# Kernel optimization log

Hardware: AMD Instinct MI355X
Metric: run time of the kernel (lower is better)

## Reference

```python
import jax, jax.numpy as jnp
import numpy as np

B, C, CI, H, W = 8, 256, 64, 64, 64  # batch, in_channels, inter_channels, spatial


def conv1x1(x, w, b):
    # x: [B,C,H,W], w: [O,C] (1x1 kernel), b: [O]
    return jnp.einsum('bchw,oc->bohw', x, w) + b[None, :, None, None]


def setup_inputs() -> dict:
    key = jax.random.key(0)
    ks = jax.random.split(key, 9)
    s_in = 1.0 / np.sqrt(C)
    s_ci = 1.0 / np.sqrt(CI)
    return {
        'x': jax.random.normal(ks[0], (B, C, H, W), dtype=jnp.float32),
        'g_w': jax.random.uniform(ks[1], (CI, C), jnp.float32, -s_in, s_in),
        'g_b': jax.random.uniform(ks[2], (CI,), jnp.float32, -s_in, s_in),
        'theta_w': jax.random.uniform(ks[3], (CI, C), jnp.float32, -s_in, s_in),
        'theta_b': jax.random.uniform(ks[4], (CI,), jnp.float32, -s_in, s_in),
        'phi_w': jax.random.uniform(ks[5], (CI, C), jnp.float32, -s_in, s_in),
        'phi_b': jax.random.uniform(ks[6], (CI,), jnp.float32, -s_in, s_in),
        'w_w': jax.random.uniform(ks[7], (C, CI), jnp.float32, -s_ci, s_ci),
        'w_b': jax.random.uniform(ks[8], (C,), jnp.float32, -s_ci, s_ci),
    }


def reference(x, g_w, g_b, theta_w, theta_b, phi_w, phi_b, w_w, w_b):
    b, c, h, w = x.shape
    n = h * w
    # 1x1 conv projections, flattened over spatial positions -> [B, N, CI]
    g_x = conv1x1(x, g_w, g_b).reshape(b, CI, n).transpose(0, 2, 1)
    theta_x = conv1x1(x, theta_w, theta_b).reshape(b, CI, n).transpose(0, 2, 1)
    phi_x = conv1x1(x, phi_w, phi_b).reshape(b, CI, n)  # [B, CI, N]
    # Full non-scaled attention over spatial positions
    f = jnp.einsum('bnc,bcm->bnm', theta_x, phi_x)       # [B, N, N]
    f_div_c = jax.nn.softmax(f, axis=-1)
    y = jnp.einsum('bnm,bmc->bnc', f_div_c, g_x)         # [B, N, CI]
    y = y.transpose(0, 2, 1).reshape(b, CI, h, w)
    w_y = conv1x1(y, w_w, w_b)                            # [B, C, H, W]
    return w_y + x
```

## Files before the change

### kernel.cpp

```cpp
#include <hip/hip_runtime.h>
#include <hip/hip_bf16.h>

#define B_  8
#define C_  256
#define CI_ 64
#define N_  4096
#define KSPLIT 2
#define KTILES (N_ / 64 / KSPLIT)

typedef short short8  __attribute__((ext_vector_type(8)));
typedef short sh4     __attribute__((ext_vector_type(4)));
typedef float floatx4 __attribute__((ext_vector_type(4)));

__device__ __forceinline__ unsigned short f2bf(float f) {
    unsigned u = __builtin_bit_cast(unsigned, f);
    u += 0x7FFFu + ((u >> 16) & 1u);
    return (unsigned short)(u >> 16);
}

__device__ __forceinline__ unsigned pk2(float a, float b) {
#if __has_builtin(__builtin_amdgcn_cvt_pk_bf16_f32)
    auto r = __builtin_amdgcn_cvt_pk_bf16_f32(a, b);
    return __builtin_bit_cast(unsigned, r);
#else
    return (unsigned)f2bf(a) | ((unsigned)f2bf(b) << 16);
#endif
}

__device__ __forceinline__ floatx4 mfma32(short8 a, short8 b, floatx4 c) {
    return __builtin_amdgcn_mfma_f32_16x16x32_bf16(a, b, c, 0, 0, 0);
}
__device__ __forceinline__ floatx4 mfma16(sh4 a, sh4 b, floatx4 c) {
#if __has_builtin(__builtin_amdgcn_mfma_f32_16x16x16bf16_1k)
    return __builtin_amdgcn_mfma_f32_16x16x16bf16_1k(a, b, c, 0, 0, 0);
#else
    floatx4 d;
    asm("v_mfma_f32_16x16x16_bf16 %0, %1, %2, %3" : "=v"(d) : "v"(a), "v"(b), "v"(c));
    return d;
#endif
}

__global__ __launch_bounds__(256) void proj_kernel(
    const float* __restrict__ x,
    const float* __restrict__ wg, const float* __restrict__ bg,
    const float* __restrict__ wt, const float* __restrict__ bt,
    const float* __restrict__ wp, const float* __restrict__ bp,
    unsigned short* __restrict__ gws,
    unsigned short* __restrict__ tws,
    unsigned short* __restrict__ pws)
{
    constexpr int WS = 40;
    constexpr int GS = 72;
    __shared__ __align__(16) unsigned short wsl[2][192 * WS];
    __shared__ __align__(16) unsigned short gt[64 * GS];

    const int t    = threadIdx.x;
    const int lane = t & 63;
    const int w    = t >> 6;
    const int l15  = lane & 15;
    const int quad = lane >> 4;
    const int n0   = blockIdx.x * 64;
    const int b    = blockIdx.y;

    floatx4 acc[12];
#pragma unroll
    for (int ot = 0; ot < 12; ++ot) { floatx4 z = {0.f, 0.f, 0.f, 0.f}; acc[ot] = z; }

    const int nA = n0 + w * 16 + l15;
    const float* xbase = x + (size_t)b * C_ * N_ + nA;

#pragma unroll
    for (int it = 0; it < 6; ++it) {
        int u = t + it * 256;
        int row = u >> 3, c4 = u & 7;
        const float* src = (row < 64)  ? (wg + row * C_)
                         : (row < 128) ? (wt + (row - 64) * C_)
                                       : (wp + (row - 128) * C_);
        float4 v = *(const float4*)(src + c4 * 4);
        uint2 uu = { pk2(v.x, v.y), pk2(v.z, v.w) };
        *(uint2*)&wsl[0][row * WS + c4 * 4] = uu;
    }
    float xv[8];
#pragma unroll
    for (int j = 0; j < 8; ++j) xv[j] = xbase[(size_t)(quad * 8 + j) * N_];
    __syncthreads();

    for (int kk = 0; kk < 8; ++kk) {
        uint4 au = { pk2(xv[0], xv[1]), pk2(xv[2], xv[3]),
                     pk2(xv[4], xv[5]), pk2(xv[6], xv[7]) };
        short8 af = __builtin_bit_cast(short8, au);

        float nx[8];
        if (kk < 7) {
#pragma unroll
            for (int j = 0; j < 8; ++j)
                nx[j] = xbase[(size_t)((kk + 1) * 32 + quad * 8 + j) * N_];
#pragma unroll
            for (int it = 0; it < 6; ++it) {
                int u = t + it * 256;
                int row = u >> 3, c4 = u & 7;
                const float* src = (row < 64)  ? (wg + row * C_)
                                 : (row < 128) ? (wt + (row - 64) * C_)
                                               : (wp + (row - 128) * C_);
                float4 v = *(const float4*)(src + (kk + 1) * 32 + c4 * 4);
                uint2 uu = { pk2(v.x, v.y), pk2(v.z, v.w) };
                *(uint2*)&wsl[(kk + 1) & 1][row * WS + c4 * 4] = uu;
            }
        }

#pragma unroll
        for (int ot = 0; ot < 12; ++ot) {
            short8 bf = *(const short8*)&wsl[kk & 1][(ot * 16 + l15) * WS + quad * 8];
            acc[ot] = mfma32(af, bf, acc[ot]);
        }
        __syncthreads();
#pragma unroll
        for (int j = 0; j < 8; ++j) xv[j] = nx[j];
    }

#pragma unroll
    for (int ot = 0; ot < 12; ++ot) {
        const int oc = ot * 16 + l15;
        const float bias = (ot < 4) ? bg[oc] : (ot < 8) ? bt[oc - 64] : bp[oc - 128];
        if (ot < 4) {
#pragma unroll
            for (int r = 0; r < 4; ++r)
                gt[oc * GS + w * 16 + quad * 4 + r] = f2bf(acc[ot][r] + bias);
        } else {
            unsigned short* dst = (ot < 8) ? tws : pws;
            const int ci = (ot < 8) ? (oc - 64) : (oc - 128);
#pragma unroll
            for (int r = 0; r < 4; ++r) {
                int n = n0 + w * 16 + quad * 4 + r;
                dst[((size_t)b * N_ + n) * CI_ + ci] = f2bf(acc[ot][r] + bias);
            }
        }
    }
    __syncthreads();
#pragma unroll
    for (int it = 0; it < 2; ++it) {
        int u = t + it * 256;
        int ci = u >> 3, n8 = u & 7;
        uint4 v = *(const uint4*)&gt[ci * GS + n8 * 8];
        *(uint4*)(gws + ((size_t)b * CI_ + ci) * N_ + n0 + n8 * 8) = v;
    }
}

__global__ __launch_bounds__(256, 4) void attn_kernel(
    const unsigned short* __restrict__ gws,
    const unsigned short* __restrict__ tws,
    const unsigned short* __restrict__ pws,
    float* __restrict__ Opart,
    float* __restrict__ lpart)
{
    constexpr int LDW = 72;
    __shared__ __align__(16) unsigned short Ks[2][64 * LDW];
    __shared__ __align__(16) unsigned short Vs[2][64 * LDW];

    const int t    = threadIdx.x;
    const int lane = t & 63;
    const int w    = t >> 6;
    const int l15  = lane & 15;
    const int quad = lane >> 4;
    const int b    = blockIdx.x;
    const int q0   = blockIdx.y * 64;
    const int sp   = blockIdx.z;

    const int srow = t >> 3;
    const int sc8  = t & 7;

    const uint4* kbase = (const uint4*)(pws + ((size_t)b * N_ + sp * (N_ / KSPLIT)) * CI_);
    const unsigned short* vbase =
        gws + ((size_t)b * CI_ + srow) * N_ + sp * (N_ / KSPLIT) + sc8 * 8;

    short8 qf[2];
    {
        const unsigned short* qrow = tws + ((size_t)b * N_ + q0 + w * 16 + l15) * CI_;
        qf[0] = *(const short8*)(qrow + quad * 8);
        qf[1] = *(const short8*)(qrow + 32 + quad * 8);
    }

    {
        uint4 k0 = kbase[t];
        uint4 k1 = kbase[t + 256];
        uint4 v0 = *(const uint4*)(vbase);
        uint4 v1 = *(const uint4*)(vbase + 32 * N_);
        *(uint4*)&Ks[0][srow * LDW + sc8 * 8]        = k0;
        *(uint4*)&Ks[0][(srow + 32) * LDW + sc8 * 8] = k1;
        *(uint4*)&Vs[0][srow * LDW + sc8 * 8]        = v0;
        *(uint4*)&Vs[0][(srow + 32) * LDW + sc8 * 8] = v1;
    }
    __syncthreads();

    sh4 ones4;
#pragma unroll
    for (int j = 0; j < 4; ++j) ones4[j] = (short)0x3F80;

    floatx4 Oacc[4], lacc;
    { floatx4 z = {0.f, 0.f, 0.f, 0.f}; lacc = z;
#pragma unroll
      for (int f = 0; f < 4; ++f) Oacc[f] = z; }

    const float LOG2E = 1.4426950408889634f;

    for (int j = 0; j < KTILES; ++j) {
        const int p  = j & 1;
        const int jn = (j + 1) & (KTILES - 1);

        uint4 pk0 = kbase[jn * 512 + t];
        uint4 pk1 = kbase[jn * 512 + t + 256];
        uint4 pv0 = *(const uint4*)(vbase + jn * 64);
        uint4 pv1 = *(const uint4*)(vbase + 32 * N_ + jn * 64);

        floatx4 s[4];
#pragma unroll
        for (int f = 0; f < 4; ++f) {
            floatx4 z = {0.f, 0.f, 0.f, 0.f};
            s[f] = z;
#pragma unroll
            for (int ks = 0; ks < 2; ++ks) {
                short8 ka = *(const short8*)&Ks[p][(f * 16 + l15) * LDW + ks * 32 + quad * 8];
                s[f] = mfma32(ka, qf[ks], s[f]);
            }
        }

        sh4 pfr[4];
#pragma unroll
        for (int f = 0; f < 4; ++f) {
            uint2 uu = { pk2(__builtin_amdgcn_exp2f(s[f][0] * LOG2E),
                             __builtin_amdgcn_exp2f(s[f][1] * LOG2E)),
                         pk2(__builtin_amdgcn_exp2f(s[f][2] * LOG2E),
                             __builtin_amdgcn_exp2f(s[f][3] * LOG2E)) };
            pfr[f] = __builtin_bit_cast(sh4, uu);
        }

#pragma unroll
        for (int f = 0; f < 4; ++f) {
            lacc = mfma16(pfr[f], ones4, lacc);
#pragma unroll
            for (int fc = 0; fc < 4; ++fc) {
                sh4 vb = *(const sh4*)&Vs[p][(fc * 16 + l15) * LDW + f * 16 + quad * 4];
                Oacc[fc] = mfma16(pfr[f], vb, Oacc[fc]);
            }
        }

        *(uint4*)&Ks[1 - p][srow * LDW + sc8 * 8]        = pk0;
        *(uint4*)&Ks[1 - p][(srow + 32) * LDW + sc8 * 8] = pk1;
        *(uint4*)&Vs[1 - p][srow * LDW + sc8 * 8]        = pv0;
        *(uint4*)&Vs[1 - p][(srow + 32) * LDW + sc8 * 8] = pv1;

        __syncthreads();
    }

#pragma unroll
    for (int r = 0; r < 4; ++r) {
        int row = q0 + w * 16 + quad * 4 + r;
        size_t obase = ((size_t)(sp * B_ + b) * N_ + row) * CI_;
#pragma unroll
        for (int fc = 0; fc < 4; ++fc)
            Opart[obase + fc * 16 + l15] = Oacc[fc][r];
        if (l15 == 0)
            lpart[(size_t)(sp * B_ + b) * N_ + row] = lacc[r];
    }
}

__global__ __launch_bounds__(256) void out_kernel(
    const float* __restrict__ Opart,
    const float* __restrict__ lpart,
    const float* __restrict__ ww,
    const float* __restrict__ wb,
    const float* __restrict__ x,
    float* __restrict__ out)
{
    constexpr int WS = 72;
    __shared__ __align__(16) unsigned short wws[C_ * WS];

    const int t    = threadIdx.x;
    const int lane = t & 63;
    const int w    = t >> 6;
    const int l15  = lane & 15;
    const int quad = lane >> 4;
    const int n0   = blockIdx.x * 64;
    const int b    = blockIdx.y;

#pragma unroll
    for (int it = 0; it < 16; ++it) {
        int u = t + it * 256;
        int row = u >> 4, c4 = u & 15;
        float4 v = *(const float4*)(ww + row * CI_ + c4 * 4);
        uint2 uu = { pk2(v.x, v.y), pk2(v.z, v.w) };
        *(uint2*)&wws[row * WS + c4 * 4] = uu;
    }
    __syncthreads();

    floatx4 acc[16];
#pragma unroll
    for (int ot = 0; ot < 16; ++ot) { floatx4 z = {0.f, 0.f, 0.f, 0.f}; acc[ot] = z; }

    const int nB = n0 + w * 16 + l15;
    const float l0 = lpart[(size_t)b * N_ + nB];
    const float l1 = lpart[(size_t)(B_ + b) * N_ + nB];
    const float inv = 1.f / (l0 + l1);

#pragma unroll
    for (int ks = 0; ks < 2; ++ks) {
        const float4* o0 = (const float4*)(Opart + ((size_t)b * N_ + nB) * CI_ + ks * 32 + quad * 8);
        const float4* o1 = (const float4*)(Opart + ((size_t)(B_ + b) * N_ + nB) * CI_ + ks * 32 + quad * 8);
        float4 a0 = o0[0], a1 = o0[1];
        float4 b0 = o1[0], b1 = o1[1];
        float y0 = (a0.x + b0.x) * inv, y1 = (a0.y + b0.y) * inv;
        float y2 = (a0.z + b0.z) * inv, y3 = (a0.w + b0.w) * inv;
        float y4 = (a1.x + b1.x) * inv, y5 = (a1.y + b1.y) * inv;
        float y6 = (a1.z + b1.z) * inv, y7 = (a1.w + b1.w) * inv;
        uint4 bu = { pk2(y0, y1), pk2(y2, y3), pk2(y4, y5), pk2(y6, y7) };
        short8 bfrag = __builtin_bit_cast(short8, bu);
#pragma unroll
        for (int ot = 0; ot < 16; ++ot) {
            short8 afrag = *(const short8*)&wws[(ot * 16 + l15) * WS + ks * 32 + quad * 8];
            acc[ot] = mfma32(afrag, bfrag, acc[ot]);
        }
    }

#pragma unroll
    for (int ot = 0; ot < 16; ++ot) {
#pragma unroll
        for (int r = 0; r < 4; ++r) {
            int c = ot * 16 + quad * 4 + r;
            size_t idx = ((size_t)b * C_ + c) * N_ + n0 + w * 16 + l15;
            out[idx] = acc[ot][r] + wb[c] + x[idx];
        }
    }
}

extern "C" void kernel_launch(void* const* d_in, const int* in_sizes, int n_in,
                              void* d_out, int out_size, void* d_ws, size_t ws_size,
                              hipStream_t stream) {
    const float* x  = (const float*)d_in[0];
    const float* gw = (const float*)d_in[1];
    const float* gb = (const float*)d_in[2];
    const float* tw = (const float*)d_in[3];
    const float* tb = (const float*)d_in[4];
    const float* pw = (const float*)d_in[5];
    const float* pb = (const float*)d_in[6];
    const float* ww = (const float*)d_in[7];
    const float* wb = (const float*)d_in[8];
    float* out = (float*)d_out;

    char* ws = (char*)d_ws;
    unsigned short* gws   = (unsigned short*)(ws);
    unsigned short* tws   = (unsigned short*)(ws + (4  << 20));
    unsigned short* pws   = (unsigned short*)(ws + (8  << 20));
    float*          Opart = (float*)        (ws + (12 << 20));
    float*          lpart = (float*)        (ws + (28 << 20));

    proj_kernel<<<dim3(64, 8), 256, 0, stream>>>(x, gw, gb, tw, tb, pw, pb, gws, tws, pws);
    attn_kernel<<<dim3(8, 64, KSPLIT), 256, 0, stream>>>(gws, tws, pws, Opart, lpart);
    out_kernel<<<dim3(64, 8), 256, 0, stream>>>(Opart, lpart, ww, wb, x, out);
}
```

Before: 198.3 us.

## Restructure attention tiling, fold log2e into theta, widen proj and out grids

Several changes land at once. The key split goes from 2 to 4, and each attention block now covers 128 queries, two 16-row groups per wave, so every K and V fragment is reused twice. K fragments are read straight from global memory instead of being staged in LDS. The log2(e) scale is folded into the theta weights and bias, which removes a multiply per score. The projection kernel moves to 512 threads with output tiles split across waves, and the output kernel splits channels across two blocks and sums four partials. Together these aim to raise occupancy and data reuse, at the cost of more partial-sum traffic and uncached direct K loads.

Measured after the change: 194.4 us. No clear change (-2.0%).

```diff
diff --git a/kernel.cpp b/kernel.cpp
--- a/kernel.cpp
+++ b/kernel.cpp
@@ -5,12 +5,14 @@
 #define C_  256
 #define CI_ 64
 #define N_  4096
-#define KSPLIT 2
+#define KSPLIT 4
 #define KTILES (N_ / 64 / KSPLIT)
 
 typedef short short8  __attribute__((ext_vector_type(8)));
 typedef short sh4     __attribute__((ext_vector_type(4)));
 typedef float floatx4 __attribute__((ext_vector_type(4)));
+
+#define LOG2E 1.4426950408889634f
 
 __device__ __forceinline__ unsigned short f2bf(float f) {
     unsigned u = __builtin_bit_cast(unsigned, f);
@@ -40,7 +42,7 @@
 #endif
 }
 
-__global__ __launch_bounds__(256) void proj_kernel(
+__global__ __launch_bounds__(512, 4) void proj_kernel(
     const float* __restrict__ x,
     const float* __restrict__ wg, const float* __restrict__ bg,
     const float* __restrict__ wt, const float* __restrict__ bt,
@@ -57,27 +59,30 @@
     const int t    = threadIdx.x;
     const int lane = t & 63;
     const int w    = t >> 6;
+    const int nf   = w >> 1;
+    const int oh   = w & 1;
     const int l15  = lane & 15;
     const int quad = lane >> 4;
     const int n0   = blockIdx.x * 64;
     const int b    = blockIdx.y;
 
-    floatx4 acc[12];
-#pragma unroll
-    for (int ot = 0; ot < 12; ++ot) { floatx4 z = {0.f, 0.f, 0.f, 0.f}; acc[ot] = z; }
-
-    const int nA = n0 + w * 16 + l15;
+    floatx4 acc[6];
+#pragma unroll
+    for (int i = 0; i < 6; ++i) { floatx4 z = {0.f, 0.f, 0.f, 0.f}; acc[i] = z; }
+
+    const int nA = n0 + nf * 16 + l15;
     const float* xbase = x + (size_t)b * C_ * N_ + nA;
 
 #pragma unroll
-    for (int it = 0; it < 6; ++it) {
-        int u = t + it * 256;
+    for (int it = 0; it < 3; ++it) {
+        int u = t + it * 512;
         int row = u >> 3, c4 = u & 7;
         const float* src = (row < 64)  ? (wg + row * C_)
                          : (row < 128) ? (wt + (row - 64) * C_)
                                        : (wp + (row - 128) * C_);
+        const float sc = (row >= 64 && row < 128) ? LOG2E : 1.0f;
         float4 v = *(const float4*)(src + c4 * 4);
-        uint2 uu = { pk2(v.x, v.y), pk2(v.z, v.w) };
+        uint2 uu = { pk2(v.x * sc, v.y * sc), pk2(v.z * sc, v.w * sc) };
         *(uint2*)&wsl[0][row * WS + c4 * 4] = uu;
     }
     float xv[8];
@@ -96,22 +101,24 @@
             for (int j = 0; j < 8; ++j)
                 nx[j] = xbase[(size_t)((kk + 1) * 32 + quad * 8 + j) * N_];
 #pragma unroll
-            for (int it = 0; it < 6; ++it) {
-                int u = t + it * 256;
+            for (int it = 0; it < 3; ++it) {
+                int u = t + it * 512;
                 int row = u >> 3, c4 = u & 7;
                 const float* src = (row < 64)  ? (wg + row * C_)
                                  : (row < 128) ? (wt + (row - 64) * C_)
                                                : (wp + (row - 128) * C_);
+                const float sc = (row >= 64 && row < 128) ? LOG2E : 1.0f;
                 float4 v = *(const float4*)(src + (kk + 1) * 32 + c4 * 4);
-                uint2 uu = { pk2(v.x, v.y), pk2(v.z, v.w) };
+                uint2 uu = { pk2(v.x * sc, v.y * sc), pk2(v.z * sc, v.w * sc) };
                 *(uint2*)&wsl[(kk + 1) & 1][row * WS + c4 * 4] = uu;
             }
         }
 
 #pragma unroll
-        for (int ot = 0; ot < 12; ++ot) {
+        for (int oti = 0; oti < 6; ++oti) {
+            const int ot = oh * 6 + oti;
             short8 bf = *(const short8*)&wsl[kk & 1][(ot * 16 + l15) * WS + quad * 8];
-            acc[ot] = mfma32(af, bf, acc[ot]);
+            acc[oti] = mfma32(af, bf, acc[oti]);
         }
         __syncthreads();
 #pragma unroll
@@ -119,28 +126,29 @@
     }
 
 #pragma unroll
-    for (int ot = 0; ot < 12; ++ot) {
+    for (int oti = 0; oti < 6; ++oti) {
+        const int ot = oh * 6 + oti;
         const int oc = ot * 16 + l15;
-        const float bias = (ot < 4) ? bg[oc] : (ot < 8) ? bt[oc - 64] : bp[oc - 128];
+        const float bias = (ot < 4) ? bg[oc]
+                         : (ot < 8) ? bt[oc - 64] * LOG2E
+                                    : bp[oc - 128];
         if (ot < 4) {
 #pragma unroll
             for (int r = 0; r < 4; ++r)
-                gt[oc * GS + w * 16 + quad * 4 + r] = f2bf(acc[ot][r] + bias);
+                gt[oc * GS + nf * 16 + quad * 4 + r] = f2bf(acc[oti][r] + bias);
         } else {
             unsigned short* dst = (ot < 8) ? tws : pws;
             const int ci = (ot < 8) ? (oc - 64) : (oc - 128);
 #pragma unroll
             for (int r = 0; r < 4; ++r) {
-                int n = n0 + w * 16 + quad * 4 + r;
-                dst[((size_t)b * N_ + n) * CI_ + ci] = f2bf(acc[ot][r] + bias);
+                int n = n0 + nf * 16 + quad * 4 + r;
+                dst[((size_t)b * N_ + n) * CI_ + ci] = f2bf(acc[oti][r] + bias);
             }
         }
     }
     __syncthreads();
-#pragma unroll
-    for (int it = 0; it < 2; ++it) {
-        int u = t + it * 256;
-        int ci = u >> 3, n8 = u & 7;
+    {
+        int ci = t >> 3, n8 = t & 7;
         uint4 v = *(const uint4*)&gt[ci * GS + n8 * 8];
         *(uint4*)(gws + ((size_t)b * CI_ + ci) * N_ + n0 + n8 * 8) = v;
     }
@@ -154,7 +162,6 @@
     float* __restrict__ lpart)
 {
     constexpr int LDW = 72;
-    __shared__ __align__(16) unsigned short Ks[2][64 * LDW];
     __shared__ __align__(16) unsigned short Vs[2][64 * LDW];
 
     const int t    = threadIdx.x;
@@ -163,30 +170,28 @@
     const int l15  = lane & 15;
     const int quad = lane >> 4;
     const int b    = blockIdx.x;
-    const int q0   = blockIdx.y * 64;
+    const int q0   = blockIdx.y * 128;
     const int sp   = blockIdx.z;
 
     const int srow = t >> 3;
     const int sc8  = t & 7;
 
-    const uint4* kbase = (const uint4*)(pws + ((size_t)b * N_ + sp * (N_ / KSPLIT)) * CI_);
-    const unsigned short* vbase =
+    const unsigned short* kslice = pws + ((size_t)b * N_ + sp * (N_ / KSPLIT)) * CI_;
+    const unsigned short* vbase  =
         gws + ((size_t)b * CI_ + srow) * N_ + sp * (N_ / KSPLIT) + sc8 * 8;
 
-    short8 qf[2];
+    short8 qf[2][2];
+#pragma unroll
+    for (int qg = 0; qg < 2; ++qg) {
+        const unsigned short* qrow =
+            tws + ((size_t)b * N_ + q0 + w * 32 + qg * 16 + l15) * CI_;
+        qf[qg][0] = *(const short8*)(qrow + quad * 8);
+        qf[qg][1] = *(const short8*)(qrow + 32 + quad * 8);
+    }
+
     {
-        const unsigned short* qrow = tws + ((size_t)b * N_ + q0 + w * 16 + l15) * CI_;
-        qf[0] = *(const short8*)(qrow + quad * 8);
-        qf[1] = *(const short8*)(qrow + 32 + quad * 8);
-    }
-
-    {
-        uint4 k0 = kbase[t];
-        uint4 k1 = kbase[t + 256];
         uint4 v0 = *(const uint4*)(vbase);
         uint4 v1 = *(const uint4*)(vbase + 32 * N_);
-        *(uint4*)&Ks[0][srow * LDW + sc8 * 8]        = k0;
-        *(uint4*)&Ks[0][(srow + 32) * LDW + sc8 * 8] = k1;
         *(uint4*)&Vs[0][srow * LDW + sc8 * 8]        = v0;
         *(uint4*)&Vs[0][(srow + 32) * LDW + sc8 * 8] = v1;
     }
@@ -196,56 +201,50 @@
 #pragma unroll
     for (int j = 0; j < 4; ++j) ones4[j] = (short)0x3F80;
 
-    floatx4 Oacc[4], lacc;
-    { floatx4 z = {0.f, 0.f, 0.f, 0.f}; lacc = z;
-#pragma unroll
-      for (int f = 0; f < 4; ++f) Oacc[f] = z; }
-
-    const float LOG2E = 1.4426950408889634f;
+    floatx4 Oacc[2][4], lacc[2];
+    { floatx4 z = {0.f, 0.f, 0.f, 0.f};
+      lacc[0] = z; lacc[1] = z;
+#pragma unroll
+      for (int qg = 0; qg < 2; ++qg)
+#pragma unroll
+          for (int f = 0; f < 4; ++f) Oacc[qg][f] = z; }
 
     for (int j = 0; j < KTILES; ++j) {
         const int p  = j & 1;
         const int jn = (j + 1) & (KTILES - 1);
 
-        uint4 pk0 = kbase[jn * 512 + t];
-        uint4 pk1 = kbase[jn * 512 + t + 256];
         uint4 pv0 = *(const uint4*)(vbase + jn * 64);
         uint4 pv1 = *(const uint4*)(vbase + 32 * N_ + jn * 64);
 
-        floatx4 s[4];
+        const unsigned short* kt = kslice + (size_t)j * 64 * CI_;
+
 #pragma unroll
         for (int f = 0; f < 4; ++f) {
-            floatx4 z = {0.f, 0.f, 0.f, 0.f};
-            s[f] = z;
-#pragma unroll
-            for (int ks = 0; ks < 2; ++ks) {
-                short8 ka = *(const short8*)&Ks[p][(f * 16 + l15) * LDW + ks * 32 + quad * 8];
-                s[f] = mfma32(ka, qf[ks], s[f]);
+            short8 ka0 = *(const short8*)(kt + (f * 16 + l15) * CI_ + quad * 8);
+            short8 ka1 = *(const short8*)(kt + (f * 16 + l15) * CI_ + 32 + quad * 8);
+
+            sh4 pfr[2];
+#pragma unroll
+            for (int qg = 0; qg < 2; ++qg) {
+                floatx4 s = {0.f, 0.f, 0.f, 0.f};
+                s = mfma32(ka0, qf[qg][0], s);
+                s = mfma32(ka1, qf[qg][1], s);
+                uint2 uu = { pk2(__builtin_amdgcn_exp2f(s[0]),
+                                 __builtin_amdgcn_exp2f(s[1])),
+                             pk2(__builtin_amdgcn_exp2f(s[2]),
+                                 __builtin_amdgcn_exp2f(s[3])) };
+                pfr[qg] = __builtin_bit_cast(sh4, uu);
+                lacc[qg] = mfma16(pfr[qg], ones4, lacc[qg]);
             }
-        }
-
-        sh4 pfr[4];
-#pragma unroll
-        for (int f = 0; f < 4; ++f) {
-            uint2 uu = { pk2(__builtin_amdgcn_exp2f(s[f][0] * LOG2E),
-                             __builtin_amdgcn_exp2f(s[f][1] * LOG2E)),
-                         pk2(__builtin_amdgcn_exp2f(s[f][2] * LOG2E),
-                             __builtin_amdgcn_exp2f(s[f][3] * LOG2E)) };
-            pfr[f] = __builtin_bit_cast(sh4, uu);
-        }
-
-#pragma unroll
-        for (int f = 0; f < 4; ++f) {
-            lacc = mfma16(pfr[f], ones4, lacc);
 #pragma unroll
             for (int fc = 0; fc < 4; ++fc) {
                 sh4 vb = *(const sh4*)&Vs[p][(fc * 16 + l15) * LDW + f * 16 + quad * 4];
-                Oacc[fc] = mfma16(pfr[f], vb, Oacc[fc]);
+#pragma unroll
+                for (int qg = 0; qg < 2; ++qg)
+                    Oacc[qg][fc] = mfma16(pfr[qg], vb, Oacc[qg][fc]);
             }
         }
 
-        *(uint4*)&Ks[1 - p][srow * LDW + sc8 * 8]        = pk0;
-        *(uint4*)&Ks[1 - p][(srow + 32) * LDW + sc8 * 8] = pk1;
         *(uint4*)&Vs[1 - p][srow * LDW + sc8 * 8]        = pv0;
         *(uint4*)&Vs[1 - p][(srow + 32) * LDW + sc8 * 8] = pv1;
 
@@ -253,18 +252,21 @@
     }
 
 #pragma unroll
-    for (int r = 0; r < 4; ++r) {
-        int row = q0 + w * 16 + quad * 4 + r;
-        size_t obase = ((size_t)(sp * B_ + b) * N_ + row) * CI_;
-#pragma unroll
-        for (int fc = 0; fc < 4; ++fc)
-            Opart[obase + fc * 16 + l15] = Oacc[fc][r];
-        if (l15 == 0)
-            lpart[(size_t)(sp * B_ + b) * N_ + row] = lacc[r];
-    }
-}
-
-__global__ __launch_bounds__(256) void out_kernel(
+    for (int qg = 0; qg < 2; ++qg) {
+#pragma unroll
+        for (int r = 0; r < 4; ++r) {
+            int row = q0 + w * 32 + qg * 16 + quad * 4 + r;
+            size_t obase = ((size_t)(sp * B_ + b) * N_ + row) * CI_;
+#pragma unroll
+            for (int fc = 0; fc < 4; ++fc)
+                Opart[obase + fc * 16 + l15] = Oacc[qg][fc][r];
+            if (l15 == 0)
+                lpart[(size_t)(sp * B_ + b) * N_ + row] = lacc[qg][r];
+        }
+    }
+}
+
+__global__ __launch_bounds__(256, 4) void out_kernel(
     const float* __restrict__ Opart,
     const float* __restrict__ lpart,
     const float* __restrict__ ww,
@@ -273,7 +275,7 @@
     float* __restrict__ out)
 {
     constexpr int WS = 72;
-    __shared__ __align__(16) unsigned short wws[C_ * WS];
+    __shared__ __align__(16) unsigned short wws[128 * WS];
 
     const int t    = threadIdx.x;
     const int lane = t & 63;
@@ -282,50 +284,57 @@
     const int quad = lane >> 4;
     const int n0   = blockIdx.x * 64;
     const int b    = blockIdx.y;
-
-#pragma unroll
-    for (int it = 0; it < 16; ++it) {
+    const int ch   = blockIdx.z;
+
+#pragma unroll
+    for (int it = 0; it < 8; ++it) {
         int u = t + it * 256;
         int row = u >> 4, c4 = u & 15;
-        float4 v = *(const float4*)(ww + row * CI_ + c4 * 4);
+        float4 v = *(const float4*)(ww + (ch * 128 + row) * CI_ + c4 * 4);
         uint2 uu = { pk2(v.x, v.y), pk2(v.z, v.w) };
         *(uint2*)&wws[row * WS + c4 * 4] = uu;
     }
     __syncthreads();
 
-    floatx4 acc[16];
-#pragma unroll
-    for (int ot = 0; ot < 16; ++ot) { floatx4 z = {0.f, 0.f, 0.f, 0.f}; acc[ot] = z; }
+    floatx4 acc[8];
+#pragma unroll
+    for (int ot = 0; ot < 8; ++ot) { floatx4 z = {0.f, 0.f, 0.f, 0.f}; acc[ot] = z; }
 
     const int nB = n0 + w * 16 + l15;
-    const float l0 = lpart[(size_t)b * N_ + nB];
-    const float l1 = lpart[(size_t)(B_ + b) * N_ + nB];
-    const float inv = 1.f / (l0 + l1);
+    float lsum = 0.f;
+#pragma unroll
+    for (int sp = 0; sp < KSPLIT; ++sp)
+        lsum += lpart[(size_t)(sp * B_ + b) * N_ + nB];
+    const float inv = 1.f / lsum;
 
 #pragma unroll
     for (int ks = 0; ks < 2; ++ks) {
-        const float4* o0 = (const float4*)(Opart + ((size_t)b * N_ + nB) * CI_ + ks * 32 + quad * 8);
-        const float4* o1 = (const float4*)(Opart + ((size_t)(B_ + b) * N_ + nB) * CI_ + ks * 32 + quad * 8);
-        float4 a0 = o0[0], a1 = o0[1];
-        float4 b0 = o1[0], b1 = o1[1];
-        float y0 = (a0.x + b0.x) * inv, y1 = (a0.y + b0.y) * inv;
-        float y2 = (a0.z + b0.z) * inv, y3 = (a0.w + b0.w) * inv;
-        float y4 = (a1.x + b1.x) * inv, y5 = (a1.y + b1.y) * inv;
-        float y6 = (a1.z + b1.z) * inv, y7 = (a1.w + b1.w) * inv;
-        uint4 bu = { pk2(y0, y1), pk2(y2, y3), pk2(y4, y5), pk2(y6, y7) };
+        float ysum[8] = {0.f, 0.f, 0.f, 0.f, 0.f, 0.f, 0.f, 0.f};
+#pragma unroll
+        for (int sp = 0; sp < KSPLIT; ++sp) {
+            const float4* o = (const float4*)(Opart +
+                ((size_t)(sp * B_ + b) * N_ + nB) * CI_ + ks * 32 + quad * 8);
+            float4 a0 = o[0], a1 = o[1];
+            ysum[0] += a0.x; ysum[1] += a0.y; ysum[2] += a0.z; ysum[3] += a0.w;
+            ysum[4] += a1.x; ysum[5] += a1.y; ysum[6] += a1.z; ysum[7] += a1.w;
+        }
+        uint4 bu = { pk2(ysum[0] * inv, ysum[1] * inv),
+                     pk2(ysum[2] * inv, ysum[3] * inv),
+                     pk2(ysum[4] * inv, ysum[5] * inv),
+                     pk2(ysum[6] * inv, ysum[7] * inv) };
         short8 bfrag = __builtin_bit_cast(short8, bu);
 #pragma unroll
-        for (int ot = 0; ot < 16; ++ot) {
+        for (int ot = 0; ot < 8; ++ot) {
             short8 afrag = *(const short8*)&wws[(ot * 16 + l15) * WS + ks * 32 + quad * 8];
             acc[ot] = mfma32(afrag, bfrag, acc[ot]);
         }
     }
 
 #pragma unroll
-    for (int ot = 0; ot < 16; ++ot) {
+    for (int ot = 0; ot < 8; ++ot) {
 #pragma unroll
         for (int r = 0; r < 4; ++r) {
-            int c = ot * 16 + quad * 4 + r;
+            int c = ch * 128 + ot * 16 + quad * 4 + r;
             size_t idx = ((size_t)b * C_ + c) * N_ + n0 + w * 16 + l15;
             out[idx] = acc[ot][r] + wb[c] + x[idx];
         }
@@ -351,9 +360,9 @@
     unsigned short* tws   = (unsigned short*)(ws + (4  << 20));
     unsigned short* pws   = (unsigned short*)(ws + (8  << 20));
     float*          Opart = (float*)        (ws + (12 << 20));
-    float*          lpart = (float*)        (ws + (28 << 20));
-
-    proj_kernel<<<dim3(64, 8), 256, 0, stream>>>(x, gw, gb, tw, tb, pw, pb, gws, tws, pws);
-    attn_kernel<<<dim3(8, 64, KSPLIT), 256, 0, stream>>>(gws, tws, pws, Opart, lpart);
-    out_kernel<<<dim3(64, 8), 256, 0, stream>>>(Opart, lpart, ww, wb, x, out);
-}
+    float*          lpart = (float*)        (ws + (44 << 20));
+
+    proj_kernel<<<dim3(64, 8), 512, 0, stream>>>(x, gw, gb, tw, tb, pw, pb, gws, tws, pws);
+    attn_kernel<<<dim3(8, 32, KSPLIT), 256, 0, stream>>>(gws, tws, pws, Opart, lpart);
+    out_kernel<<<dim3(64, 8, 2), 256, 0, stream>>>(Opart, lpart, ww, wb, x, out);
+}
```
